# Optimization experiments

Measured on AMD Instinct MI355X. Metric: run time of the kernel, lower is better.

Reference implementation:

```python
import jax, jax.numpy as jnp
import numpy as np


def setup_inputs() -> dict:
    key = jax.random.key(0)
    kq, kk, kv = jax.random.split(key, 3)
    B, H, SQ, KV, D = 2, 16, 2048, 4096, 128
    q = jax.random.normal(kq, (B, H, SQ, D), dtype=jnp.float32)
    k = jax.random.normal(kk, (B, H, KV, D), dtype=jnp.float32)
    v = jax.random.normal(kv, (B, H, KV, D), dtype=jnp.float32)
    return {"q": q, "k": k, "v": v}


def reference(q, k, v):
    # Faithful to F.scaled_dot_product_attention with a boolean mask that is
    # True for the first half of KV positions (masked positions -> -inf).
    KV = k.shape[2]
    D = q.shape[-1]
    scale = 1.0 / jnp.sqrt(jnp.asarray(D, dtype=q.dtype))
    # [B, H, Sq, KV] scores
    scores = jnp.einsum("bhqd,bhkd->bhqk", q, k) * scale
    kv_pos = jnp.arange(KV)
    mask = (kv_pos < KV // 2)[None, None, None, :]  # [1,1,1,KV]
    neg_inf = jnp.asarray(jnp.finfo(scores.dtype).min, dtype=scores.dtype)
    scores = jnp.where(mask, scores, neg_inf)
    attn = jax.nn.softmax(scores, axis=-1)
    return jnp.einsum("bhqk,bhkd->bhqd", attn, v)
```

## Files before the change

### kernel.cpp

```cpp
#include <hip/hip_runtime.h>


#define NT 32

typedef _Float16 half8  __attribute__((ext_vector_type(8)));
typedef __fp16   fp16x2 __attribute__((ext_vector_type(2)));
typedef float    floatx4 __attribute__((ext_vector_type(4)));
typedef unsigned int uint;
typedef uint     uintx4 __attribute__((ext_vector_type(4)));

#if __has_builtin(__builtin_amdgcn_exp2f)
#define EXP2(x) __builtin_amdgcn_exp2f(x)
#else
#define EXP2(x) exp2f(x)
#endif

union H2U { fp16x2 h; uint u; };
union H8U { uint u[4]; half8 h; };

static __device__ __forceinline__ uint pk(float a, float b) {
    H2U z; z.h = __builtin_amdgcn_cvt_pkrtz(a, b); return z.u;
}

#define KH_BH 524288u
#define VT_BASE 16777216u
#define VT_BH 524288u

#define GLOAD_LDS16(g, l)                                                     \
    __builtin_amdgcn_global_load_lds(                                         \
        (const __attribute__((address_space(1))) uint*)(const void*)(g),      \
        (__attribute__((address_space(3))) uint*)(void*)(l), 16, 0, 0)

__global__ __launch_bounds__(256)
void cvt_kernel(const float* __restrict__ K, const float* __restrict__ V,
                char* __restrict__ ws) {
    const int bid = blockIdx.x;
    const int bh  = bid >> 5;
    const int kv0 = (bid & 31) * 64;
    const int t   = threadIdx.x;

    const float* Kb = K + (size_t)bh * 4096 * 128 + (size_t)kv0 * 128;
    const float* Vb = V + (size_t)bh * 4096 * 128 + (size_t)kv0 * 128;
    char* Khb = ws + (size_t)bh * KH_BH + (size_t)kv0 * 256;
    char* Vtb = ws + VT_BASE + (size_t)bh * VT_BH;

    {
        const int c16 = t & 15;
        #pragma unroll
        for (int rnd = 0; rnd < 4; ++rnd) {
            const int r = rnd * 16 + (t >> 4);
            const float* src = Kb + (size_t)r * 128 + c16 * 8;
            floatx4 a = *(const floatx4*)src;
            floatx4 b = *(const floatx4*)(src + 4);
            H8U hh;
            hh.u[0] = pk(a[0], a[1]); hh.u[1] = pk(a[2], a[3]);
            hh.u[2] = pk(b[0], b[1]); hh.u[3] = pk(b[2], b[3]);
            const int key = (r & 7) ^ ((r >> 1) & 4);
            *(half8*)(Khb + r * 256 + 16 * (c16 ^ key)) = hh.h;
        }
    }

    __shared__ __align__(16) uint U[128 * 32];
    {
        const int dpos = t & 31;
        const int k3   = t >> 5;
        #pragma unroll
        for (int rnd = 0; rnd < 4; ++rnd) {
            const int kvp = rnd * 8 + k3;
            floatx4 a = *(const floatx4*)(Vb + (size_t)(2 * kvp) * 128 + 4 * dpos);
            floatx4 b = *(const floatx4*)(Vb + (size_t)(2 * kvp + 1) * 128 + 4 * dpos);
            #pragma unroll
            for (int e = 0; e < 4; ++e) {
                const int d   = 4 * dpos + e;
                const int col = (kvp & 3) | ((((kvp >> 2) ^ d) & 7) << 2);
                U[d * 32 + col] = pk(a[e], b[e]);
            }
        }
    }
    __syncthreads();
    {
        const int s = t & 7;
        #pragma unroll
        for (int rnd = 0; rnd < 4; ++rnd) {
            const int d = rnd * 32 + (t >> 3);
            uintx4 u = *(const uintx4*)&U[d * 32 + 4 * s];
            *(uintx4*)(Vtb + (size_t)d * 4096 + (size_t)kv0 * 2 + 16 * s) = u;
        }
    }
}

__global__ __launch_bounds__(512, 4)
void fa_kernel(const float* __restrict__ Q, float* __restrict__ O,
               const char* __restrict__ ws) {
    const float SCALE = 0.08838834764831845f * 1.4426950408889634f;

    __shared__ __align__(16) char smem[66560];

    const int t    = threadIdx.x;
    const int lane = t & 63;
    const int w    = t >> 6;
    const int wq   = w & 3;
    const int h    = w >> 2;
    const int c    = lane & 15;
    const int qd   = lane >> 4;

    const int idx  = blockIdx.x;
    const int xcd  = idx & 7;
    const int slot = idx >> 3;
    const int qt   = slot & 15;
    const int bh   = xcd + 8 * (slot >> 4);
    const int q0   = qt * 128;

    const float* Qb  = Q + (size_t)bh * 2048 * 128;
    float*       Ob  = O + (size_t)bh * 2048 * 128;
    const char*  Khb = ws + (size_t)bh * KH_BH;
    const char*  Vtb = ws + VT_BASE + (size_t)bh * VT_BH;

    char* const kb0 = smem;
    char* const vb0 = smem + 32768;

    half8 bq[2][4];
    #pragma unroll
    for (int m = 0; m < 2; ++m) {
        #pragma unroll
        for (int s = 0; s < 4; ++s) {
            const int row = q0 + 32 * wq + 16 * m + c;
            const float* p = Qb + (size_t)row * 128 + 32 * s + 8 * qd;
            floatx4 x = *(const floatx4*)p;
            floatx4 y = *(const floatx4*)(p + 4);
            H8U hh;
            hh.u[0] = pk(x[0] * SCALE, x[1] * SCALE);
            hh.u[1] = pk(x[2] * SCALE, x[3] * SCALE);
            hh.u[2] = pk(y[0] * SCALE, y[1] * SCALE);
            hh.u[3] = pk(y[2] * SCALE, y[3] * SCALE);
            bq[m][s] = hh.h;
        }
    }

    floatx4 o[2][8];
    float lsum[2] = {0.f, 0.f};
    #pragma unroll
    for (int m = 0; m < 2; ++m)
        #pragma unroll
        for (int dt = 0; dt < 8; ++dt) o[m][dt] = (floatx4){0.f, 0.f, 0.f, 0.f};

    #define ISSUE_K(kv0_, dst_)                                                  \
        { _Pragma("unroll")                                                      \
          for (int j = 0; j < 2; ++j) {                                          \
              const int i = 2 * w + j;                                           \
              const char* g = Khb + (size_t)(kv0_) * 256 +                       \
                              (size_t)(4 * i + (lane >> 4)) * 256 + (lane & 15) * 16; \
              GLOAD_LDS16(g, (dst_) + i * 1024); } }
    #define ISSUE_V(kv0_, dst_)                                                  \
        { _Pragma("unroll")                                                      \
          for (int j = 0; j < 2; ++j) {                                          \
              const int i = 2 * w + j;                                           \
              const char* g = Vtb + (size_t)(8 * i + (lane >> 3)) * 4096 +       \
                              (size_t)(kv0_) * 2 + (lane & 7) * 16;              \
              GLOAD_LDS16(g, (dst_) + i * 1024); } }

    ISSUE_K(0, kb0);
    ISSUE_V(0, vb0);
    __syncthreads();

    for (int kt = 0; kt < NT; ++kt) {
        const int cur = kt & 1;
        char* kcur = kb0 + cur * 16384;
        char* vcur = vb0 + cur * 16384;
        if (kt + 1 < NT) {
            ISSUE_K((kt + 1) * 64, kb0 + (1 - cur) * 16384);
            ISSUE_V((kt + 1) * 64, vb0 + (1 - cur) * 16384);
        }

        floatx4 st[2][2];
        #pragma unroll
        for (int g = 0; g < 2; ++g)
            #pragma unroll
            for (int m = 0; m < 2; ++m) st[g][m] = (floatx4){0.f, 0.f, 0.f, 0.f};

        __builtin_amdgcn_s_setprio(1);
        #pragma unroll
        for (int g = 0; g < 2; ++g) {
            const int row = 32 * h + 8 * (c >> 2) + 4 * g + (c & 3);
            const int key = (row & 7) ^ ((row >> 1) & 4);
            #pragma unroll
            for (int s = 0; s < 4; ++s) {
                half8 ka = *(const half8*)(kcur + row * 256 + 16 * ((4 * s + qd) ^ key));
                st[g][0] = __builtin_amdgcn_mfma_f32_16x16x32_f16(ka, bq[0][s], st[g][0], 0, 0, 0);
                st[g][1] = __builtin_amdgcn_mfma_f32_16x16x32_f16(ka, bq[1][s], st[g][1], 0, 0, 0);
            }
        }
        __builtin_amdgcn_s_setprio(0);

        half8 pb[2];
        #pragma unroll
        for (int m = 0; m < 2; ++m) {
            const float p0 = EXP2(st[0][m][0]);
            const float p1 = EXP2(st[0][m][1]);
            const float p2 = EXP2(st[0][m][2]);
            const float p3 = EXP2(st[0][m][3]);
            const float p4 = EXP2(st[1][m][0]);
            const float p5 = EXP2(st[1][m][1]);
            const float p6 = EXP2(st[1][m][2]);
            const float p7 = EXP2(st[1][m][3]);
            lsum[m] += ((p0 + p1) + (p2 + p3)) + ((p4 + p5) + (p6 + p7));
            H8U hh;
            hh.u[0] = pk(p0, p1); hh.u[1] = pk(p2, p3);
            hh.u[2] = pk(p4, p5); hh.u[3] = pk(p6, p7);
            pb[m] = hh.h;
        }

        __builtin_amdgcn_s_setprio(1);
        #pragma unroll
        for (int dt = 0; dt < 8; ++dt) {
            const int d = 16 * dt + c;
            half8 va = *(const half8*)(vcur + d * 128 + 16 * ((4 * h + qd) ^ (d & 7)));
            o[0][dt] = __builtin_amdgcn_mfma_f32_16x16x32_f16(va, pb[0], o[0][dt], 0, 0, 0);
            o[1][dt] = __builtin_amdgcn_mfma_f32_16x16x32_f16(va, pb[1], o[1][dt], 0, 0, 0);
        }
        __builtin_amdgcn_s_setprio(0);

        __syncthreads();
    }

    #pragma unroll
    for (int m = 0; m < 2; ++m) {
        lsum[m] += __shfl_xor(lsum[m], 16, 64);
        lsum[m] += __shfl_xor(lsum[m], 32, 64);
    }
    float* lbuf = (float*)(smem + 65536);
    if (qd == 0) {
        lbuf[h * 128 + 32 * wq + c]      = lsum[0];
        lbuf[h * 128 + 32 * wq + 16 + c] = lsum[1];
    }
    floatx4* obuf = (floatx4*)smem;
    if (h == 1) {
        #pragma unroll
        for (int m = 0; m < 2; ++m)
            #pragma unroll
            for (int dt = 0; dt < 8; ++dt)
                obuf[(m * 8 + dt) * 256 + wq * 64 + lane] = o[m][dt];
    }
    __syncthreads();
    if (h == 0) {
        #pragma unroll
        for (int m = 0; m < 2; ++m) {
            const int qrow = 32 * wq + 16 * m + c;
            const float invl = 1.0f / (lbuf[qrow] + lbuf[128 + qrow]);
            #pragma unroll
            for (int dt = 0; dt < 8; ++dt) {
                floatx4 r = o[m][dt] + obuf[(m * 8 + dt) * 256 + wq * 64 + lane];
                r[0] *= invl; r[1] *= invl; r[2] *= invl; r[3] *= invl;
                *(floatx4*)&Ob[(size_t)(q0 + qrow) * 128 + 16 * dt + 4 * qd] = r;
            }
        }
    }
}

extern "C" void kernel_launch(void* const* d_in, const int* in_sizes, int n_in,
                              void* d_out, int out_size, void* d_ws, size_t ws_size,
                              hipStream_t stream) {
    const float* q = (const float*)d_in[0];
    const float* k = (const float*)d_in[1];
    const float* v = (const float*)d_in[2];
    float* out = (float*)d_out;
    char* ws = (char*)d_ws;
    cvt_kernel<<<dim3(1024), dim3(256), 0, stream>>>(k, v, ws);
    fa_kernel<<<dim3(512), dim3(512), 0, stream>>>(q, out, ws);
}
```

Before: 275.5 us.

## Split PV output over head dimension with LDS exchange of P between sibling waves

Instead of each half of the waves computing a partial O over its own KV half for all 128 output dims and reducing at the end, each wave now owns half of the head dimension. It gets its sibling's P fragments through an LDS exchange guarded by an extra barrier per tile. This halves the O accumulator registers and removes the final cross-wave O reduction. It adds a barrier and LDS traffic in every iteration. The V transpose layout swizzle is also changed to match the new read pattern.

```diff
diff --git a/kernel.cpp b/kernel.cpp
--- a/kernel.cpp
+++ b/kernel.cpp
@@ -72,7 +72,8 @@
             #pragma unroll
             for (int e = 0; e < 4; ++e) {
                 const int d   = 4 * dpos + e;
-                const int col = (kvp & 3) | ((((kvp >> 2) ^ d) & 7) << 2);
+                const int col = (kvp & 3) |
+                                ((((kvp >> 2) ^ d ^ (d >> 2)) & 7) << 2);
                 U[d * 32 + col] = pk(a[e], b[e]);
             }
         }
@@ -84,7 +85,8 @@
         for (int rnd = 0; rnd < 4; ++rnd) {
             const int d = rnd * 32 + (t >> 3);
             uintx4 u = *(const uintx4*)&U[d * 32 + 4 * s];
-            *(uintx4*)(Vtb + (size_t)d * 4096 + (size_t)kv0 * 2 + 16 * s) = u;
+            *(uintx4*)(Vtb + (size_t)d * 4096 + (size_t)kv0 * 2 +
+                       16 * ((s ^ (d >> 2)) & 7)) = u;
         }
     }
 }
@@ -94,13 +96,13 @@
                const char* __restrict__ ws) {
     const float SCALE = 0.08838834764831845f * 1.4426950408889634f;
 
-    __shared__ __align__(16) char smem[66560];
+    __shared__ __align__(16) char smem[81920];
 
     const int t    = threadIdx.x;
     const int lane = t & 63;
     const int w    = t >> 6;
     const int wq   = w & 3;
-    const int h    = w >> 2;
+    const int dh   = w >> 2;
     const int c    = lane & 15;
     const int qd   = lane >> 4;
 
@@ -118,6 +120,7 @@
 
     char* const kb0 = smem;
     char* const vb0 = smem + 32768;
+    char* const pex = smem + 65536;
 
     half8 bq[2][4];
     #pragma unroll
@@ -137,12 +140,12 @@
         }
     }
 
-    floatx4 o[2][8];
+    floatx4 o[2][4];
     float lsum[2] = {0.f, 0.f};
     #pragma unroll
     for (int m = 0; m < 2; ++m)
         #pragma unroll
-        for (int dt = 0; dt < 8; ++dt) o[m][dt] = (floatx4){0.f, 0.f, 0.f, 0.f};
+        for (int dt = 0; dt < 4; ++dt) o[m][dt] = (floatx4){0.f, 0.f, 0.f, 0.f};
 
     #define ISSUE_K(kv0_, dst_)                                                  \
         { _Pragma("unroll")                                                      \
@@ -159,6 +162,9 @@
                               (size_t)(kv0_) * 2 + (lane & 7) * 16;              \
               GLOAD_LDS16(g, (dst_) + i * 1024); } }
 
+    char* const pex_own = pex + (((w & 7)) << 11) + (qd << 8) + (c << 4);
+    const char* const pex_sib = pex + ((w ^ 4) << 11) + (qd << 8) + (c << 4);
+
     ISSUE_K(0, kb0);
     ISSUE_V(0, vb0);
     __syncthreads();
@@ -181,7 +187,7 @@
         __builtin_amdgcn_s_setprio(1);
         #pragma unroll
         for (int g = 0; g < 2; ++g) {
-            const int row = 32 * h + 8 * (c >> 2) + 4 * g + (c & 3);
+            const int row = 32 * dh + 8 * (c >> 2) + 4 * g + (c & 3);
             const int key = (row & 7) ^ ((row >> 1) & 4);
             #pragma unroll
             for (int s = 0; s < 4; ++s) {
@@ -210,13 +216,26 @@
             pb[m] = hh.h;
         }
 
+        *(half8*)(pex_own)        = pb[0];
+        *(half8*)(pex_own + 1024) = pb[1];
+
+        asm volatile("s_waitcnt lgkmcnt(0)" ::: "memory");
+        __builtin_amdgcn_s_barrier();
+        asm volatile("" ::: "memory");
+
+        half8 ps0 = *(const half8*)(pex_sib);
+        half8 ps1 = *(const half8*)(pex_sib + 1024);
+
         __builtin_amdgcn_s_setprio(1);
         #pragma unroll
-        for (int dt = 0; dt < 8; ++dt) {
-            const int d = 16 * dt + c;
-            half8 va = *(const half8*)(vcur + d * 128 + 16 * ((4 * h + qd) ^ (d & 7)));
-            o[0][dt] = __builtin_amdgcn_mfma_f32_16x16x32_f16(va, pb[0], o[0][dt], 0, 0, 0);
-            o[1][dt] = __builtin_amdgcn_mfma_f32_16x16x32_f16(va, pb[1], o[1][dt], 0, 0, 0);
+        for (int dt = 0; dt < 4; ++dt) {
+            const int d = 64 * dh + 16 * dt + c;
+            half8 va_own = *(const half8*)(vcur + d * 128 + 16 * ((4 * dh + qd) ^ (d & 7)));
+            half8 va_sib = *(const half8*)(vcur + d * 128 + 16 * ((4 * (dh ^ 1) + qd) ^ (d & 7)));
+            o[0][dt] = __builtin_amdgcn_mfma_f32_16x16x32_f16(va_own, pb[0], o[0][dt], 0, 0, 0);
+            o[1][dt] = __builtin_amdgcn_mfma_f32_16x16x32_f16(va_own, pb[1], o[1][dt], 0, 0, 0);
+            o[0][dt] = __builtin_amdgcn_mfma_f32_16x16x32_f16(va_sib, ps0, o[0][dt], 0, 0, 0);
+            o[1][dt] = __builtin_amdgcn_mfma_f32_16x16x32_f16(va_sib, ps1, o[1][dt], 0, 0, 0);
         }
         __builtin_amdgcn_s_setprio(0);
 
@@ -228,31 +247,21 @@
         lsum[m] += __shfl_xor(lsum[m], 16, 64);
         lsum[m] += __shfl_xor(lsum[m], 32, 64);
     }
-    float* lbuf = (float*)(smem + 65536);
+    float* lbuf = (float*)pex;
     if (qd == 0) {
-        lbuf[h * 128 + 32 * wq + c]      = lsum[0];
-        lbuf[h * 128 + 32 * wq + 16 + c] = lsum[1];
-    }
-    floatx4* obuf = (floatx4*)smem;
-    if (h == 1) {
-        #pragma unroll
-        for (int m = 0; m < 2; ++m)
-            #pragma unroll
-            for (int dt = 0; dt < 8; ++dt)
-                obuf[(m * 8 + dt) * 256 + wq * 64 + lane] = o[m][dt];
+        lbuf[dh * 128 + 32 * wq + c]      = lsum[0];
+        lbuf[dh * 128 + 32 * wq + 16 + c] = lsum[1];
     }
     __syncthreads();
-    if (h == 0) {
-        #pragma unroll
-        for (int m = 0; m < 2; ++m) {
-            const int qrow = 32 * wq + 16 * m + c;
-            const float invl = 1.0f / (lbuf[qrow] + lbuf[128 + qrow]);
-            #pragma unroll
-            for (int dt = 0; dt < 8; ++dt) {
-                floatx4 r = o[m][dt] + obuf[(m * 8 + dt) * 256 + wq * 64 + lane];
-                r[0] *= invl; r[1] *= invl; r[2] *= invl; r[3] *= invl;
-                *(floatx4*)&Ob[(size_t)(q0 + qrow) * 128 + 16 * dt + 4 * qd] = r;
-            }
+    #pragma unroll
+    for (int m = 0; m < 2; ++m) {
+        const int qrow = 32 * wq + 16 * m + c;
+        const float invl = 1.0f / (lbuf[qrow] + lbuf[128 + qrow]);
+        #pragma unroll
+        for (int dt = 0; dt < 4; ++dt) {
+            floatx4 r = o[m][dt];
+            r[0] *= invl; r[1] *= invl; r[2] *= invl; r[3] *= invl;
+            *(floatx4*)&Ob[(size_t)(q0 + qrow) * 128 + 64 * dh + 16 * dt + 4 * qd] = r;
         }
     }
 }
```

New measurement: 232.5 us. 1.19x faster.
